# Kernel tuning notes

Measured on AMD Instinct MI355X. Metric: run time of the kernel, lower is better.

The kernel has to match this reference:

```python
import jax, jax.numpy as jnp
import numpy as np

N, IN_DIM, ENC_DIM, K = 16384, 1024, 256, 8192


def setup_inputs() -> dict:
    key = jax.random.key(0)
    ks = jax.random.split(key, 10)
    s = 0.02
    return {
        "x": jax.random.normal(ks[0], (N, IN_DIM), dtype=jnp.float32),
        "enc_w1": jax.random.normal(ks[1], (IN_DIM, ENC_DIM), dtype=jnp.float32) * s,
        "enc_b1": jnp.zeros((ENC_DIM,), dtype=jnp.float32),
        "enc_w2": jax.random.normal(ks[2], (ENC_DIM, ENC_DIM), dtype=jnp.float32) * s,
        "enc_b2": jnp.zeros((ENC_DIM,), dtype=jnp.float32),
        "codewords": jax.random.normal(ks[3], (K, ENC_DIM), dtype=jnp.float32),
        "dec_w1": jax.random.normal(ks[4], (ENC_DIM, ENC_DIM), dtype=jnp.float32) * s,
        "dec_b1": jnp.zeros((ENC_DIM,), dtype=jnp.float32),
        "dec_w2": jax.random.normal(ks[5], (ENC_DIM, IN_DIM), dtype=jnp.float32) * s,
        "dec_b2": jnp.zeros((IN_DIM,), dtype=jnp.float32),
    }


def reference(x, enc_w1, enc_b1, enc_w2, enc_b2, codewords, dec_w1, dec_b1, dec_w2, dec_b2):
    # Encoder: Linear -> ReLU -> Linear -> ReLU
    h = jax.nn.relu(x @ enc_w1 + enc_b1)
    encoded = jax.nn.relu(h @ enc_w2 + enc_b2)  # [N, ENC_DIM]

    # VQ: full Euclidean distance matrix (torch.cdist, p=2), argmin, gather
    x2 = jnp.sum(encoded * encoded, axis=1, keepdims=True)          # [N, 1]
    c2 = jnp.sum(codewords * codewords, axis=1)                     # [K]
    d2 = x2 + c2[None, :] - 2.0 * (encoded @ codewords.T)           # [N, K]
    distances = jnp.sqrt(jnp.maximum(d2, 0.0))
    quantized_indices = jnp.argmin(distances, axis=1)               # [N] int
    quantized_distances = jnp.take_along_axis(
        distances, quantized_indices[:, None], axis=1)[:, 0]        # [N]
    quantized = codewords[quantized_indices]                        # [N, ENC_DIM]

    # Decoder: Linear -> ReLU -> Linear
    g = jax.nn.relu(quantized @ dec_w1 + dec_b1)
    reconstructed = g @ dec_w2 + dec_b2                              # [N, IN_DIM]
    return quantized_indices, quantized_distances, reconstructed, quantized
```

## Files before the change

kernel.cpp:

```cpp
#include <hip/hip_runtime.h>
#include <hip/hip_bf16.h>

#define NROWS   16384
#define IN_DIM  1024
#define ENC_DIM 256
#define KCW     8192
#define NCB     32

typedef __attribute__((ext_vector_type(8))) short short8v;
typedef __attribute__((ext_vector_type(4))) float f32x4;
typedef unsigned long long u64;
typedef unsigned int u32;

__device__ __forceinline__ unsigned short f2bf_rne(float x) {
    unsigned u = __float_as_uint(x);
    unsigned r = (u + 0x7fffu + ((u >> 16) & 1u)) >> 16;
    return (unsigned short)r;
}
__device__ __forceinline__ float bf2f(unsigned short h) {
    return __uint_as_float(((unsigned)h) << 16);
}
__device__ __forceinline__ int lex_lt(float d, int i, float D, int I) {
    return (d < D) || (d == D && i < I);
}
__device__ __forceinline__ void t2mrg(u64& b1, u64& b2, u64 c1, u64 c2) {
    u64 hi = (b1 > c1) ? b1 : c1;
    u64 lo2 = (b2 < c2) ? b2 : c2;
    b1 = (b1 < c1) ? b1 : c1;
    b2 = (hi < lo2) ? hi : lo2;
}
__device__ __forceinline__ void gload16(const void* g, void* l) {
    __builtin_amdgcn_global_load_lds(
        (__attribute__((address_space(1))) void*)g,
        (__attribute__((address_space(3))) void*)l, 16, 0, 0);
}

template<int K>
__device__ __forceinline__ void tsplit_body(const float* __restrict__ W,
                                            unsigned short* __restrict__ Wt,
                                            int Ncols, int idx) {
    int n = idx / (K / 4), k4 = (idx % (K / 4)) * 4;
    float vx = W[(size_t)(k4 + 0) * Ncols + n];
    float vy = W[(size_t)(k4 + 1) * Ncols + n];
    float vz = W[(size_t)(k4 + 2) * Ncols + n];
    float vw = W[(size_t)(k4 + 3) * Ncols + n];
    ushort4 hi, lo;
    hi.x = f2bf_rne(vx); lo.x = f2bf_rne(vx - bf2f(hi.x));
    hi.y = f2bf_rne(vy); lo.y = f2bf_rne(vy - bf2f(hi.y));
    hi.z = f2bf_rne(vz); lo.z = f2bf_rne(vz - bf2f(hi.z));
    hi.w = f2bf_rne(vw); lo.w = f2bf_rne(vw - bf2f(hi.w));
    const int m = (n & 7) << 4;
    char* rp = (char*)(Wt + (size_t)n * (2 * K));
    int bh = k4 * 2, bl = (K + k4) * 2;
    *(ushort4*)(rp + ((bh & ~127) | ((bh & 127) ^ m))) = hi;
    *(ushort4*)(rp + ((bl & ~127) | ((bl & 127) ^ m))) = lo;
}

__global__ __launch_bounds__(256)
void prep_all(const float* __restrict__ ew1, const float* __restrict__ ew2,
              const float* __restrict__ dw1, const float* __restrict__ dw2,
              const float* __restrict__ cw,
              unsigned short* __restrict__ w1ts, unsigned short* __restrict__ ew2t,
              unsigned short* __restrict__ dw1t, unsigned short* __restrict__ dw2t,
              unsigned short* __restrict__ Be,   float* __restrict__ c2) {
    int idx = blockIdx.x * 256 + threadIdx.x;
    if (idx < 65536)        { tsplit_body<1024>(ew1, w1ts, 256, idx); }
    else if (idx < 81920)   { tsplit_body<256>(ew2, ew2t, 256, idx - 65536); }
    else if (idx < 98304)   { tsplit_body<256>(dw1, dw1t, 256, idx - 81920); }
    else if (idx < 163840)  { tsplit_body<256>(dw2, dw2t, 1024, idx - 98304); }
    else if (idx < 688128) {
        int e = idx - 163840;
        int row = e >> 6, kq = (e & 63) * 4;
        float4 v = ((const float4*)cw)[e];
        ushort4 hi, lo;
        hi.x = f2bf_rne(v.x); lo.x = f2bf_rne(v.x - bf2f(hi.x));
        hi.y = f2bf_rne(v.y); lo.y = f2bf_rne(v.y - bf2f(hi.y));
        hi.z = f2bf_rne(v.z); lo.z = f2bf_rne(v.z - bf2f(hi.z));
        hi.w = f2bf_rne(v.w); lo.w = f2bf_rne(v.w - bf2f(hi.w));
        const int m = (row & 7) << 4;
        char* rowp = (char*)(Be + (size_t)row * 512);
        int bh = kq * 2, bl = (256 + kq) * 2;
        *(ushort4*)(rowp + ((bh & ~127) | ((bh & 127) ^ m))) = hi;
        *(ushort4*)(rowp + ((bl & ~127) | ((bl & 127) ^ m))) = lo;
        float s = (v.x * v.x + v.y * v.y) + (v.z * v.z + v.w * v.w);
#pragma unroll
        for (int off = 1; off < 64; off <<= 1) s += __shfl_xor(s, off);
        if ((threadIdx.x & 63) == 0) c2[row] = s;
    }
}

struct MMP {
    const unsigned short* A;
    const unsigned short* Bt;
    const float* bias;
    float* C;
    unsigned short* Cs;
    int N, ars, brs, crs, KQ, EPI, gx;
};

__device__ void mm_device512(const MMP p, int bx, int by, int tid, char* lds) {
    unsigned short (*As)[64] = (unsigned short(*)[64])lds;
    unsigned short (*Bs)[64] = (unsigned short(*)[64])(lds + 16384);
    const int lane = tid & 63;
    const int wid = tid >> 6;
    const int wr = wid >> 2, wc = wid & 3;
    const int brow = by * 128;
    const int bcol = bx * 128;
    const int K = p.KQ * 64;

    f32x4 acc[4][2] = {};

    const int fr = tid >> 3;
    const int fk = (tid & 7) * 8;
    const int swz = (lane & 7) << 4;
    const int arow = wr * 64 + (lane & 15);
    const int brw  = wc * 32 + (lane & 15);
    const int klane = (lane >> 4) * 16;

    bool first = true;
#pragma unroll
    for (int term = 0; term < 3; ++term) {
        const int kaT = (term == 2) ? K : 0;
        const int kbT = (term == 1) ? K : 0;
        for (int kq = 0; kq < p.KQ; ++kq) {
            if (!first) __syncthreads();
            first = false;
            const int ka0 = kaT + kq * 64;
            const int kb0 = kbT + kq * 64;
#pragma unroll
            for (int l = 0; l < 2; ++l) {
                gload16(p.A  + (size_t)(brow + l * 64 + fr) * p.ars + ka0 + fk,
                        (char*)&As[0][0] + l * 8192 + tid * 16);
                gload16(p.Bt + (size_t)(bcol + l * 64 + fr) * p.brs + kb0 + fk,
                        (char*)&Bs[0][0] + l * 8192 + tid * 16);
            }
            __syncthreads();
#pragma unroll
            for (int kk = 0; kk < 2; ++kk) {
                const int kb = (kk * 64 + klane) ^ swz;
                short8v af[4], bfv[2];
#pragma unroll
                for (int mi = 0; mi < 4; mi++)
                    af[mi] = *(const short8v*)((const char*)&As[arow + mi * 16][0] + kb);
#pragma unroll
                for (int ni = 0; ni < 2; ni++)
                    bfv[ni] = *(const short8v*)((const char*)&Bs[brw + ni * 16][0] + kb);
#pragma unroll
                for (int mi = 0; mi < 4; mi++)
#pragma unroll
                    for (int ni = 0; ni < 2; ni++)
                        acc[mi][ni] = __builtin_amdgcn_mfma_f32_16x16x32_bf16(
                            af[mi], bfv[ni], acc[mi][ni], 0, 0, 0);
            }
        }
    }

#pragma unroll
    for (int mi = 0; mi < 4; mi++) {
#pragma unroll
        for (int q = 0; q < 4; q++) {
            int row = brow + wr * 64 + mi * 16 + (lane >> 4) * 4 + q;
            const int m = (row & 7) << 4;
            char* rp = (char*)(p.Cs + (size_t)row * p.crs);
#pragma unroll
            for (int ni = 0; ni < 2; ni++) {
                int col = bcol + wc * 32 + ni * 16 + (lane & 15);
                float v = acc[mi][ni][q] + p.bias[col];
                if (p.EPI != 3) v = fmaxf(v, 0.f);
                if (p.EPI & 1) p.C[(size_t)row * p.N + col] = v;
                if (p.EPI != 3) {
                    unsigned short hi = f2bf_rne(v);
                    int bh = col * 2;
                    *(unsigned short*)(rp + ((bh & ~127) | ((bh & 127) ^ m))) = hi;
                    if (p.EPI == 2) {
                        unsigned short lo = f2bf_rne(v - bf2f(hi));
                        int bl = (256 + col) * 2;
                        *(unsigned short*)(rp + ((bl & ~127) | ((bl & 127) ^ m))) = lo;
                    }
                }
            }
        }
    }
}

__global__ __launch_bounds__(512)
void mm_one(MMP p) {
    __shared__ __align__(16) char pool[32768];
    mm_device512(p, blockIdx.x % p.gx, blockIdx.x / p.gx, threadIdx.x, pool);
}

__global__ __launch_bounds__(512)
void enc1_fused(const float* __restrict__ x,
                const unsigned short* __restrict__ w1ts,
                const float* __restrict__ bias,
                unsigned short* __restrict__ Hs) {
    __shared__ __align__(16) unsigned short Ah[64][64];
    __shared__ __align__(16) unsigned short Al[64][64];
    __shared__ __align__(16) unsigned short Bh[256][64];
    __shared__ __align__(16) unsigned short Bl[256][64];
    const int tid = threadIdx.x;
    const int lane = tid & 63;
    const int wid = tid >> 6;
    const int wr = wid >> 2, wc = wid & 3;
    const int brow = blockIdx.x * 64;

    f32x4 acc[2][4] = {};

    const int fr = tid >> 3;
    const int fk = (tid & 7) * 8;
    const int swz = (lane & 7) << 4;
    const int arow = wr * 32 + (lane & 15);
    const int brw  = wc * 64 + (lane & 15);
    const int klane = (lane >> 4) * 16;
    const int aoff = fr * 128 + ((fk * 2) ^ ((fr & 7) << 4));

    float4 c0, c1, n0, n1;
    {
        const float* xp = x + (size_t)(brow + fr) * 1024 + fk;
        c0 = *(const float4*)xp; c1 = *(const float4*)(xp + 4);
    }

    for (int s = 0; s < 16; ++s) {
        const int k0 = s * 64;
        if (s) __syncthreads();
        {
            float vv[8] = { c0.x, c0.y, c0.z, c0.w, c1.x, c1.y, c1.z, c1.w };
            short8v uh, ul;
#pragma unroll
            for (int i = 0; i < 8; i++) {
                unsigned short h = f2bf_rne(vv[i]);
                uh[i] = (short)h;
                ul[i] = (short)f2bf_rne(vv[i] - bf2f(h));
            }
            *(short8v*)((char*)&Ah[0][0] + aoff) = uh;
            *(short8v*)((char*)&Al[0][0] + aoff) = ul;
        }
#pragma unroll
        for (int l = 0; l < 4; ++l) {
            gload16(w1ts + (size_t)(l * 64 + fr) * 2048 + k0 + fk,
                    (char*)&Bh[0][0] + l * 8192 + tid * 16);
            gload16(w1ts + (size_t)(l * 64 + fr) * 2048 + 1024 + k0 + fk,
                    (char*)&Bl[0][0] + l * 8192 + tid * 16);
        }
        if (s + 1 < 16) {
            const float* xp = x + (size_t)(brow + fr) * 1024 + k0 + 64 + fk;
            n0 = *(const float4*)xp; n1 = *(const float4*)(xp + 4);
        }
        __syncthreads();
#pragma unroll
        for (int kk = 0; kk < 2; ++kk) {
            const int kb = (kk * 64 + klane) ^ swz;
            short8v ah[2], al[2], bh[4], bl[4];
#pragma unroll
            for (int mi = 0; mi < 2; mi++) {
                ah[mi] = *(const short8v*)((const char*)&Ah[arow + mi * 16][0] + kb);
                al[mi] = *(const short8v*)((const char*)&Al[arow + mi * 16][0] + kb);
            }
#pragma unroll
            for (int ni = 0; ni < 4; ni++) {
                bh[ni] = *(const short8v*)((const char*)&Bh[brw + ni * 16][0] + kb);
                bl[ni] = *(const short8v*)((const char*)&Bl[brw + ni * 16][0] + kb);
            }
#pragma unroll
            for (int mi = 0; mi < 2; mi++)
#pragma unroll
                for (int ni = 0; ni < 4; ni++) {
                    acc[mi][ni] = __builtin_amdgcn_mfma_f32_16x16x32_bf16(
                        ah[mi], bh[ni], acc[mi][ni], 0, 0, 0);
                    acc[mi][ni] = __builtin_amdgcn_mfma_f32_16x16x32_bf16(
                        ah[mi], bl[ni], acc[mi][ni], 0, 0, 0);
                    acc[mi][ni] = __builtin_amdgcn_mfma_f32_16x16x32_bf16(
                        al[mi], bh[ni], acc[mi][ni], 0, 0, 0);
                }
        }
        c0 = n0; c1 = n1;
    }

#pragma unroll
    for (int mi = 0; mi < 2; mi++) {
#pragma unroll
        for (int q = 0; q < 4; q++) {
            int row = brow + wr * 32 + mi * 16 + (lane >> 4) * 4 + q;
            const int m = (row & 7) << 4;
            char* rp = (char*)(Hs + (size_t)row * 512);
#pragma unroll
            for (int ni = 0; ni < 4; ni++) {
                int col = wc * 64 + ni * 16 + (lane & 15);
                float v = fmaxf(acc[mi][ni][q] + bias[col], 0.f);
                unsigned short hi = f2bf_rne(v);
                unsigned short lo = f2bf_rne(v - bf2f(hi));
                int bh_ = col * 2, bl_ = (256 + col) * 2;
                *(unsigned short*)(rp + ((bh_ & ~127) | ((bh_ & 127) ^ m))) = hi;
                *(unsigned short*)(rp + ((bl_ & ~127) | ((bl_ & 127) ^ m))) = lo;
            }
        }
    }
}

__global__ __launch_bounds__(512)
void vq_mfma(const unsigned short* __restrict__ Ae,
             const unsigned short* __restrict__ Be,
             const float* __restrict__ c2,
             ulonglong2* __restrict__ part,
             MMP pd, int nvq) {
    __shared__ __align__(16) char pool[151552];
    if ((int)blockIdx.x >= nvq) {
        int b = blockIdx.x - nvq;
        mm_device512(pd, b % pd.gx, b / pd.gx, threadIdx.x, pool);
        return;
    }
    const int tid  = threadIdx.x;
    const int lane = tid & 63;
    const int wid  = tid >> 6;
    const int wr   = wid >> 2;
    const int wc   = wid & 3;
    const int bid  = blockIdx.x;
    const int brow = (bid >> 5) * 128;
    const int bcol = (bid & 31) * 256;

    u32* s1 = (u32*)(pool + 147456);
    u32* s2 = (u32*)(pool + 149504);

    const int fr = tid >> 3;
    const int fk = (tid & 7) * 8;
    const int swz   = (lane & 7) << 4;
    const int arow  = wr * 64 + (lane & 15);
    const int brw   = wc * 64 + (lane & 15);
    const int klane = (lane >> 4) * 16;

    auto stage = [&](int s, int buf) {
        char* A = pool + buf * 49152;
        char* B = A + 16384;
        const int k0 = s * 64;
#pragma unroll
        for (int l = 0; l < 2; ++l)
            gload16(Ae + (size_t)(brow + l * 64 + fr) * 256 + k0 + fk,
                    A + l * 8192 + tid * 16);
#pragma unroll
        for (int l = 0; l < 4; ++l)
            gload16(Be + (size_t)(bcol + l * 64 + fr) * 512 + k0 + fk,
                    B + l * 8192 + tid * 16);
    };

    f32x4 acc[4][4] = {};

    stage(0, 0);
    stage(1, 1);
    asm volatile("s_waitcnt vmcnt(6)" ::: "memory");
    __builtin_amdgcn_s_barrier();

#pragma unroll
    for (int s = 0; s < 4; ++s) {
        const int buf = s % 3;
        if (s + 2 < 4) stage(s + 2, (s + 2) % 3);
        const char* A = pool + buf * 49152;
        const char* B = A + 16384;
        __builtin_amdgcn_s_setprio(1);
#pragma unroll
        for (int kk = 0; kk < 2; ++kk) {
            const int kb = (kk * 64 + klane) ^ swz;
            short8v af[4], bfv[4];
#pragma unroll
            for (int mi = 0; mi < 4; mi++)
                af[mi] = *(const short8v*)(A + (arow + mi * 16) * 128 + kb);
#pragma unroll
            for (int ni = 0; ni < 4; ni++)
                bfv[ni] = *(const short8v*)(B + (brw + ni * 16) * 128 + kb);
#pragma unroll
            for (int mi = 0; mi < 4; mi++)
#pragma unroll
                for (int ni = 0; ni < 4; ni++)
                    acc[mi][ni] = __builtin_amdgcn_mfma_f32_16x16x32_bf16(
                        bfv[ni], af[mi], acc[mi][ni], 0, 0, 0);
        }
        __builtin_amdgcn_s_setprio(0);
        if (s == 0 || s == 1) {
            asm volatile("s_waitcnt vmcnt(6)" ::: "memory");
            __builtin_amdgcn_s_barrier();
        } else if (s == 2) {
            asm volatile("s_waitcnt vmcnt(0)" ::: "memory");
            __builtin_amdgcn_s_barrier();
        }
    }

    const int qrow = lane & 15;
    const int cq   = (lane >> 4) * 4;
    float4 c2q[4];
#pragma unroll
    for (int ni = 0; ni < 4; ni++)
        c2q[ni] = *(const float4*)&c2[bcol + wc * 64 + ni * 16 + cq];

#pragma unroll
    for (int mi = 0; mi < 4; mi++) {
        u32 b1 = 0xFFFFFFFFu, b2 = 0xFFFFFFFFu;
#pragma unroll
        for (int ni = 0; ni < 4; ni++) {
            const float* cp = (const float*)&c2q[ni];
#pragma unroll
            for (int r = 0; r < 4; r++) {
                float dk = fmaf(-2.0f, acc[mi][ni][r], cp[r]);
                dk = fmaxf(dk, 0.0f);
                u32 k = (__float_as_uint(dk) & ~255u)
                      | (u32)(wc * 64 + ni * 16 + cq + r);
                u32 mx = max(k, b1);
                b1 = min(k, b1);
                b2 = min(mx, b2);
            }
        }
#pragma unroll
        for (int off = 16; off < 64; off <<= 1) {
            u32 o1 = __shfl_xor(b1, off);
            u32 o2 = __shfl_xor(b2, off);
            u32 mx = max(b1, o1);
            b1 = min(b1, o1);
            b2 = min(min(b2, o2), mx);
        }
        if (lane < 16) {
            int rl = wr * 64 + mi * 16 + qrow;
            s1[rl * 4 + wc] = b1;
            s2[rl * 4 + wc] = b2;
        }
    }
    __syncthreads();
    if (tid < 128) {
        u32 b1 = s1[tid * 4 + 0], b2 = s2[tid * 4 + 0];
#pragma unroll
        for (int w = 1; w < 4; w++) {
            u32 c1 = s1[tid * 4 + w], cc2 = s2[tid * 4 + w];
            u32 mx = max(b1, c1);
            b1 = min(b1, c1);
            b2 = min(min(b2, cc2), mx);
        }
        ulonglong2 pk;
        pk.x = ((u64)b1 << 32) | (u32)(bcol + (b1 & 255u));
        pk.y = ((u64)b2 << 32) | (u32)(bcol + (b2 & 255u));
        part[(size_t)(brow + tid) * NCB + (bid & 31)] = pk;
    }
}

__global__ __launch_bounds__(512)
void combine_dec2(const ulonglong2* __restrict__ part,
                  const float* __restrict__ enc,
                  const float* __restrict__ cw,
                  const float* __restrict__ c2,
                  float* __restrict__ outIdx,
                  float* __restrict__ outDist,
                  int* __restrict__ idx32,
                  float* __restrict__ outQ,
                  MMP pd, int nd2) {
    __shared__ __align__(16) char pool[32768];
    if ((int)blockIdx.x < nd2) {
        mm_device512(pd, blockIdx.x % pd.gx, blockIdx.x / pd.gx, threadIdx.x, pool);
        return;
    }
    const int row  = (blockIdx.x - nd2) * 8 + (threadIdx.x >> 6);
    const int lane = threadIdx.x & 63;

    u64 b1 = ~0ull, b2 = ~0ull;
    if (lane < NCB) {
        ulonglong2 pk = part[(size_t)row * NCB + lane];
        b1 = pk.x; b2 = pk.y;
    }
#pragma unroll
    for (int off = 1; off < 64; off <<= 1) {
        u64 c1 = __shfl_xor(b1, off);
        u64 cc2 = __shfl_xor(b2, off);
        t2mrg(b1, b2, c1, cc2);
    }
    int j1 = (int)(b1 & 0xffffffffu);
    int j2 = (int)(b2 & 0xffffffffu);

    float4 e4 = ((const float4*)(enc + (size_t)row * 256))[lane];
    float4 w1 = ((const float4*)(cw + (size_t)j1 * 256))[lane];
    float4 w2 = ((const float4*)(cw + (size_t)j2 * 256))[lane];
    float s1 = fmaf(e4.x, w1.x, fmaf(e4.y, w1.y, fmaf(e4.z, w1.z, e4.w * w1.w)));
    float s2 = fmaf(e4.x, w2.x, fmaf(e4.y, w2.y, fmaf(e4.z, w2.z, e4.w * w2.w)));
    float sx = (e4.x * e4.x + e4.y * e4.y) + (e4.z * e4.z + e4.w * e4.w);
#pragma unroll
    for (int off = 1; off < 64; off <<= 1) {
        s1 += __shfl_xor(s1, off);
        s2 += __shfl_xor(s2, off);
        sx += __shfl_xor(sx, off);
    }
    float d1 = sqrtf(fmaxf(sx + c2[j1] - 2.0f * s1, 0.f));
    float d2 = sqrtf(fmaxf(sx + c2[j2] - 2.0f * s2, 0.f));
    float bd; int bi;
    if (lex_lt(d1, j1, d2, j2)) { bd = d1; bi = j1; }
    else                        { bd = d2; bi = j2; }
    float4 wq = (bi == j1) ? w1 : w2;
    ((float4*)(outQ + (size_t)row * ENC_DIM))[lane] = wq;
    if (lane == 0) {
        outIdx[row]  = (float)bi;
        outDist[row] = bd;
        idx32[row]   = bi;
    }
}

__global__ void gather_rec(const int* __restrict__ idx32,
                           const float* __restrict__ rec_all,
                           float* __restrict__ outRec) {
    int row = blockIdx.x * 4 + (threadIdx.x >> 6);
    int lane = threadIdx.x & 63;
    int j = idx32[row];
    const float4* src = (const float4*)(rec_all + (size_t)j * IN_DIM);
    float4* dst = (float4*)(outRec + (size_t)row * IN_DIM);
#pragma unroll
    for (int i = 0; i < 4; i++) dst[lane + 64 * i] = src[lane + 64 * i];
}

extern "C" void kernel_launch(void* const* d_in, const int* in_sizes, int n_in,
                              void* d_out, int out_size, void* d_ws, size_t ws_size,
                              hipStream_t stream) {
    const float* x   = (const float*)d_in[0];
    const float* ew1 = (const float*)d_in[1];
    const float* eb1 = (const float*)d_in[2];
    const float* ew2 = (const float*)d_in[3];
    const float* eb2 = (const float*)d_in[4];
    const float* cw  = (const float*)d_in[5];
    const float* dw1 = (const float*)d_in[6];
    const float* db1 = (const float*)d_in[7];
    const float* dw2 = (const float*)d_in[8];
    const float* db2 = (const float*)d_in[9];
    float* out = (float*)d_out;
    float* ws  = (float*)d_ws;

    float* outIdx  = out;
    float* outDist = out + NROWS;
    float* outRec  = out + 2 * NROWS;
    float* outQ    = out + 2 * NROWS + (size_t)NROWS * IN_DIM;

    float*          enc     = ws;
    unsigned short* Ae      = (unsigned short*)(ws + 4194304);
    unsigned short* Gs      = (unsigned short*)(ws + 6291456);
    unsigned short* Hs      = (unsigned short*)(ws + 8388608);
    ulonglong2*     part    = (ulonglong2*)(ws + 8388608);
    float*          rec_all = ws + 10485760;
    unsigned short* Be      = (unsigned short*)(ws + 18874368);
    unsigned short* w1ts    = (unsigned short*)(ws + 20971520);
    unsigned short* ew2t    = (unsigned short*)(ws + 21233664);
    unsigned short* dw1t    = (unsigned short*)(ws + 21299200);
    unsigned short* dw2t    = (unsigned short*)(ws + 21364736);
    float*          c2      = ws + 21626880;
    int*            idx32   = (int*)(ws + 21635072);

    MMP p_enc2 = { Hs, ew2t, eb2, enc, Ae, 256, 512, 512, 256, 4, 1, 2 };
    MMP p_dec1 = { Be, dw1t, db1, nullptr, Gs, 256, 512, 512, 512, 4, 2, 2 };
    MMP p_dec2 = { Gs, dw2t, db2, rec_all, nullptr, 1024, 512, 512, 0, 4, 3, 8 };

    prep_all<<<2688, 256, 0, stream>>>(ew1, ew2, dw1, dw2, cw,
                                       w1ts, ew2t, dw1t, dw2t, Be, c2);
    enc1_fused<<<256, 512, 0, stream>>>(x, w1ts, eb1, Hs);
    mm_one<<<256, 512, 0, stream>>>(p_enc2);
    vq_mfma<<<4096 + 128, 512, 0, stream>>>(Ae, Be, c2, part, p_dec1, 4096);
    combine_dec2<<<512 + 2048, 512, 0, stream>>>(part, enc, cw, c2,
                                                 outIdx, outDist, idx32, outQ,
                                                 p_dec2, 512);
    gather_rec<<<NROWS / 4, 256, 0, stream>>>(idx32, rec_all, outRec);
}
```

Before: 226.8 us.

## Fuse decoder second layer with row gather and simplify VQ staging

The final decoder GEMM is no longer computed once per codeword and then copied into each output row. It is now computed directly per output row, with the A-tile loaded by gathering G rows through the chosen indices, using a three-term hi/lo bf16 split. This removes the intermediate rec_all buffer and the separate gather kernel, but doubles the decoder GEMM work (16384 rows instead of 8192) and no longer overlaps it with the combine step. Separately, the VQ distance kernel's triple-buffered asynchronous staging is replaced by a single-buffer load-sync-compute loop with smaller LDS. That may raise occupancy but exposes global load latency, and the shrunken pool must still fit the co-scheduled dec1 GEMM.

```diff
diff --git a/kernel.cpp b/kernel.cpp
--- a/kernel.cpp
+++ b/kernel.cpp
@@ -303,12 +303,17 @@
              const float* __restrict__ c2,
              ulonglong2* __restrict__ part,
              MMP pd, int nvq) {
-    __shared__ __align__(16) char pool[151552];
+    __shared__ __align__(16) char pool[53248];
     if ((int)blockIdx.x >= nvq) {
         int b = blockIdx.x - nvq;
         mm_device512(pd, b % pd.gx, b / pd.gx, threadIdx.x, pool);
         return;
     }
+    unsigned short (*As)[64] = (unsigned short(*)[64])pool;
+    unsigned short (*Bs)[64] = (unsigned short(*)[64])(pool + 16384);
+    u32* s1 = (u32*)(pool + 49152);
+    u32* s2 = (u32*)(pool + 51200);
+
     const int tid  = threadIdx.x;
     const int lane = tid & 63;
     const int wid  = tid >> 6;
@@ -318,8 +323,7 @@
     const int brow = (bid >> 5) * 128;
     const int bcol = (bid & 31) * 256;
 
-    u32* s1 = (u32*)(pool + 147456);
-    u32* s2 = (u32*)(pool + 149504);
+    f32x4 acc[4][4] = {};
 
     const int fr = tid >> 3;
     const int fk = (tid & 7) * 8;
@@ -328,58 +332,34 @@
     const int brw   = wc * 64 + (lane & 15);
     const int klane = (lane >> 4) * 16;
 
-    auto stage = [&](int s, int buf) {
-        char* A = pool + buf * 49152;
-        char* B = A + 16384;
+    for (int s = 0; s < 4; ++s) {
         const int k0 = s * 64;
+        if (s) __syncthreads();
 #pragma unroll
         for (int l = 0; l < 2; ++l)
             gload16(Ae + (size_t)(brow + l * 64 + fr) * 256 + k0 + fk,
-                    A + l * 8192 + tid * 16);
+                    (char*)&As[0][0] + l * 8192 + tid * 16);
 #pragma unroll
         for (int l = 0; l < 4; ++l)
             gload16(Be + (size_t)(bcol + l * 64 + fr) * 512 + k0 + fk,
-                    B + l * 8192 + tid * 16);
-    };
-
-    f32x4 acc[4][4] = {};
-
-    stage(0, 0);
-    stage(1, 1);
-    asm volatile("s_waitcnt vmcnt(6)" ::: "memory");
-    __builtin_amdgcn_s_barrier();
-
-#pragma unroll
-    for (int s = 0; s < 4; ++s) {
-        const int buf = s % 3;
-        if (s + 2 < 4) stage(s + 2, (s + 2) % 3);
-        const char* A = pool + buf * 49152;
-        const char* B = A + 16384;
-        __builtin_amdgcn_s_setprio(1);
+                    (char*)&Bs[0][0] + l * 8192 + tid * 16);
+        __syncthreads();
 #pragma unroll
         for (int kk = 0; kk < 2; ++kk) {
             const int kb = (kk * 64 + klane) ^ swz;
             short8v af[4], bfv[4];
 #pragma unroll
             for (int mi = 0; mi < 4; mi++)
-                af[mi] = *(const short8v*)(A + (arow + mi * 16) * 128 + kb);
+                af[mi] = *(const short8v*)((const char*)&As[arow + mi * 16][0] + kb);
 #pragma unroll
             for (int ni = 0; ni < 4; ni++)
-                bfv[ni] = *(const short8v*)(B + (brw + ni * 16) * 128 + kb);
+                bfv[ni] = *(const short8v*)((const char*)&Bs[brw + ni * 16][0] + kb);
 #pragma unroll
             for (int mi = 0; mi < 4; mi++)
 #pragma unroll
                 for (int ni = 0; ni < 4; ni++)
                     acc[mi][ni] = __builtin_amdgcn_mfma_f32_16x16x32_bf16(
                         bfv[ni], af[mi], acc[mi][ni], 0, 0, 0);
-        }
-        __builtin_amdgcn_s_setprio(0);
-        if (s == 0 || s == 1) {
-            asm volatile("s_waitcnt vmcnt(6)" ::: "memory");
-            __builtin_amdgcn_s_barrier();
-        } else if (s == 2) {
-            asm volatile("s_waitcnt vmcnt(0)" ::: "memory");
-            __builtin_amdgcn_s_barrier();
         }
     }
 
@@ -439,21 +419,15 @@
 }
 
 __global__ __launch_bounds__(512)
-void combine_dec2(const ulonglong2* __restrict__ part,
-                  const float* __restrict__ enc,
-                  const float* __restrict__ cw,
-                  const float* __restrict__ c2,
-                  float* __restrict__ outIdx,
-                  float* __restrict__ outDist,
-                  int* __restrict__ idx32,
-                  float* __restrict__ outQ,
-                  MMP pd, int nd2) {
-    __shared__ __align__(16) char pool[32768];
-    if ((int)blockIdx.x < nd2) {
-        mm_device512(pd, blockIdx.x % pd.gx, blockIdx.x / pd.gx, threadIdx.x, pool);
-        return;
-    }
-    const int row  = (blockIdx.x - nd2) * 8 + (threadIdx.x >> 6);
+void vq_combine(const ulonglong2* __restrict__ part,
+                const float* __restrict__ enc,
+                const float* __restrict__ cw,
+                const float* __restrict__ c2,
+                float* __restrict__ outIdx,
+                float* __restrict__ outDist,
+                int* __restrict__ idx32,
+                float* __restrict__ outQ) {
+    const int row  = blockIdx.x * 8 + (threadIdx.x >> 6);
     const int lane = threadIdx.x & 63;
 
     u64 b1 = ~0ull, b2 = ~0ull;
@@ -496,16 +470,92 @@
     }
 }
 
-__global__ void gather_rec(const int* __restrict__ idx32,
-                           const float* __restrict__ rec_all,
-                           float* __restrict__ outRec) {
-    int row = blockIdx.x * 4 + (threadIdx.x >> 6);
-    int lane = threadIdx.x & 63;
-    int j = idx32[row];
-    const float4* src = (const float4*)(rec_all + (size_t)j * IN_DIM);
-    float4* dst = (float4*)(outRec + (size_t)row * IN_DIM);
-#pragma unroll
-    for (int i = 0; i < 4; i++) dst[lane + 64 * i] = src[lane + 64 * i];
+__global__ __launch_bounds__(512)
+void dec2_gather(const unsigned short* __restrict__ Gs,
+                 const unsigned short* __restrict__ dw2t,
+                 const float* __restrict__ bias,
+                 const int* __restrict__ idx32,
+                 float* __restrict__ outRec) {
+    __shared__ __align__(16) unsigned short As[128][64];
+    __shared__ __align__(16) unsigned short Bs[128][64];
+    const int tid = threadIdx.x;
+    const int lane = tid & 63;
+    const int wid = tid >> 6;
+    const int wr = wid >> 2, wc = wid & 3;
+    const int bx = blockIdx.x & 7, by = blockIdx.x >> 3;
+    const int brow = by * 128;
+    const int bcol = bx * 128;
+
+    f32x4 acc[4][2] = {};
+
+    const int fr = tid >> 3;
+    const int fk = (tid & 7) * 8;
+    const int swz = (lane & 7) << 4;
+    const int arow = wr * 64 + (lane & 15);
+    const int brw  = wc * 32 + (lane & 15);
+    const int klane = (lane >> 4) * 16;
+
+    const int j0 = idx32[brow + fr];
+    const int j1r = idx32[brow + 64 + fr];
+    const int aoff0 = fr * 128 + ((fk * 2) ^ ((fr & 7) << 4));
+
+    bool first = true;
+#pragma unroll
+    for (int term = 0; term < 3; ++term) {
+        const int kaT = (term == 2) ? 256 : 0;
+        const int kbT = (term == 1) ? 256 : 0;
+        for (int kq = 0; kq < 4; ++kq) {
+            if (!first) __syncthreads();
+            first = false;
+            const int ka0 = kaT + kq * 64;
+            const int kb0 = kbT + kq * 64;
+            {
+                const char* src0 = (const char*)Gs + (size_t)j0 * 1024
+                                 + ka0 * 2 + ((fk * 2) ^ ((j0 & 7) << 4));
+                const char* src1 = (const char*)Gs + (size_t)j1r * 1024
+                                 + ka0 * 2 + ((fk * 2) ^ ((j1r & 7) << 4));
+                short8v v0 = *(const short8v*)src0;
+                short8v v1 = *(const short8v*)src1;
+                *(short8v*)((char*)&As[0][0] + aoff0) = v0;
+                *(short8v*)((char*)&As[0][0] + 8192 + aoff0) = v1;
+            }
+#pragma unroll
+            for (int l = 0; l < 2; ++l)
+                gload16(dw2t + (size_t)(bcol + l * 64 + fr) * 512 + kb0 + fk,
+                        (char*)&Bs[0][0] + l * 8192 + tid * 16);
+            __syncthreads();
+#pragma unroll
+            for (int kk = 0; kk < 2; ++kk) {
+                const int kb = (kk * 64 + klane) ^ swz;
+                short8v af[4], bfv[2];
+#pragma unroll
+                for (int mi = 0; mi < 4; mi++)
+                    af[mi] = *(const short8v*)((const char*)&As[arow + mi * 16][0] + kb);
+#pragma unroll
+                for (int ni = 0; ni < 2; ni++)
+                    bfv[ni] = *(const short8v*)((const char*)&Bs[brw + ni * 16][0] + kb);
+#pragma unroll
+                for (int mi = 0; mi < 4; mi++)
+#pragma unroll
+                    for (int ni = 0; ni < 2; ni++)
+                        acc[mi][ni] = __builtin_amdgcn_mfma_f32_16x16x32_bf16(
+                            af[mi], bfv[ni], acc[mi][ni], 0, 0, 0);
+            }
+        }
+    }
+
+#pragma unroll
+    for (int mi = 0; mi < 4; mi++) {
+#pragma unroll
+        for (int q = 0; q < 4; q++) {
+            int row = brow + wr * 64 + mi * 16 + (lane >> 4) * 4 + q;
+#pragma unroll
+            for (int ni = 0; ni < 2; ni++) {
+                int col = bcol + wc * 32 + ni * 16 + (lane & 15);
+                outRec[(size_t)row * 1024 + col] = acc[mi][ni][q] + bias[col];
+            }
+        }
+    }
 }
 
 extern "C" void kernel_launch(void* const* d_in, const int* in_sizes, int n_in,
@@ -534,7 +584,6 @@
     unsigned short* Gs      = (unsigned short*)(ws + 6291456);
     unsigned short* Hs      = (unsigned short*)(ws + 8388608);
     ulonglong2*     part    = (ulonglong2*)(ws + 8388608);
-    float*          rec_all = ws + 10485760;
     unsigned short* Be      = (unsigned short*)(ws + 18874368);
     unsigned short* w1ts    = (unsigned short*)(ws + 20971520);
     unsigned short* ew2t    = (unsigned short*)(ws + 21233664);
@@ -545,15 +594,13 @@
 
     MMP p_enc2 = { Hs, ew2t, eb2, enc, Ae, 256, 512, 512, 256, 4, 1, 2 };
     MMP p_dec1 = { Be, dw1t, db1, nullptr, Gs, 256, 512, 512, 512, 4, 2, 2 };
-    MMP p_dec2 = { Gs, dw2t, db2, rec_all, nullptr, 1024, 512, 512, 0, 4, 3, 8 };
 
     prep_all<<<2688, 256, 0, stream>>>(ew1, ew2, dw1, dw2, cw,
                                        w1ts, ew2t, dw1t, dw2t, Be, c2);
     enc1_fused<<<256, 512, 0, stream>>>(x, w1ts, eb1, Hs);
     mm_one<<<256, 512, 0, stream>>>(p_enc2);
     vq_mfma<<<4096 + 128, 512, 0, stream>>>(Ae, Be, c2, part, p_dec1, 4096);
-    combine_dec2<<<512 + 2048, 512, 0, stream>>>(part, enc, cw, c2,
-                                                 outIdx, outDist, idx32, outQ,
-                                                 p_dec2, 512);
-    gather_rec<<<NROWS / 4, 256, 0, stream>>>(idx32, rec_all, outRec);
-}
+    vq_combine<<<NROWS / 8, 512, 0, stream>>>(part, enc, cw, c2,
+                                              outIdx, outDist, idx32, outQ);
+    dec2_gather<<<1024, 512, 0, stream>>>(Gs, dw2t, db2, idx32, outRec);
+}
```

Result: slower. 236.5 us (+4.3%).
